# Performance work log

Measured on AMD Instinct MI355X. Metric: run time of the kernel, lower is better.

Reference implementation:

```python
import jax, jax.numpy as jnp
import numpy as np

N_NODES = 100000
N_EDGES = 1600000
HIDDEN = 128


def setup_inputs() -> dict:
    key = jax.random.key(0)
    k1, k2, k3, k4, k5 = jax.random.split(key, 5)
    probabilities = jax.random.uniform(k1, (N_EDGES,), dtype=jnp.float32)
    hidden = jax.random.normal(k2, (N_NODES, HIDDEN), dtype=jnp.float32)
    edge_index = jax.random.randint(k3, (2, N_EDGES), 0, N_NODES, dtype=jnp.int32)
    # nn.Linear(hidden_dim, hidden_dim): weight [out, in], bias [out]
    bound = 1.0 / np.sqrt(HIDDEN)
    lin_w = jax.random.uniform(k4, (HIDDEN, HIDDEN), minval=-bound, maxval=bound, dtype=jnp.float32)
    lin_b = jax.random.uniform(k5, (HIDDEN,), minval=-bound, maxval=bound, dtype=jnp.float32)
    return {"probabilities": probabilities, "hidden": hidden, "edge_index": edge_index,
            "lin_w": lin_w, "lin_b": lin_b}


def reference(probabilities, hidden, edge_index, lin_w, lin_b):
    # gather target-node hidden states: [E, H]
    target_hidden = hidden[edge_index[1]]
    # scale each message by its edge probability
    weighted_msg = target_hidden * probabilities[:, None]
    # scatter_add into source-node buckets: [N, H]
    aggregated = jax.ops.segment_sum(weighted_msg, edge_index[0], num_segments=hidden.shape[0])
    # trailing linear: y = aggregated @ W^T + b
    return aggregated @ lin_w.T + lin_b
```

## Files before the change

kernel.cpp:

```cpp
#include <hip/hip_runtime.h>

#define HIDDEN 128
#define NPB 64
#define CHUNK 4096
#define NBMAX 2048
#define CAP 1280

typedef __attribute__((ext_vector_type(8))) short bf16x8;
typedef __attribute__((ext_vector_type(4))) float f32x4;

static __device__ __forceinline__ ushort f2bf(float f) {
    uint u = __float_as_uint(f);
    uint r = (u + 0x7fffu + ((u >> 16) & 1u)) >> 16;
    return (ushort)r;
}

static __device__ __forceinline__ void split1(float f, ushort& h, ushort& l) {
    ushort hh = f2bf(f);
    float hf = __uint_as_float(((uint)hh) << 16);
    h = hh;
    l = f2bf(f - hf);
}

static __device__ __forceinline__ void splitt(float f, ushort& h, ushort& l) {
    uint u = __float_as_uint(f);
    h = (ushort)(u >> 16);
    l = f2bf(f - __uint_as_float(u & 0xffff0000u));
}

static __device__ __forceinline__ bf16x8 mkfrag(ushort4 a, ushort4 b) {
    bf16x8 f;
    f[0] = (short)a.x; f[1] = (short)a.y; f[2] = (short)a.z; f[3] = (short)a.w;
    f[4] = (short)b.x; f[5] = (short)b.y; f[6] = (short)b.z; f[7] = (short)b.w;
    return f;
}

__global__ __launch_bounds__(256) void bin_k(
    const int* __restrict__ ei, const float* __restrict__ prob,
    const float* __restrict__ W, int* __restrict__ gcur, int2* __restrict__ ed,
    ushort* __restrict__ wh, ushort* __restrict__ wl, int E, int NB, int HB)
{
    if ((int)blockIdx.x >= HB) {
        int i = ((int)blockIdx.x - HB) * 256 + threadIdx.x;
        ushort h, l;
        split1(W[i], h, l);
        wh[i] = h;
        wl[i] = l;
        return;
    }
    __shared__ int hist[NBMAX];
    __shared__ int base[NBMAX];
    const int t  = threadIdx.x;
    const int e0 = blockIdx.x * CHUNK;

    for (int i = t; i < NB; i += 256) hist[i] = 0;
    __syncthreads();

    int  bs[16];
    int2 pl[16];
    #pragma unroll
    for (int j = 0; j < 16; ++j) {
        int e = e0 + j * 256 + t;
        if (e < E) {
            int src = ei[e];
            int tgt = ei[E + e];
            int p15 = min((int)(prob[e] * 32768.0f + 0.5f), 32767);
            int b   = src >> 6;
            bs[j] = b;
            pl[j] = make_int2(tgt, ((src & (NPB - 1)) << 15) | p15);
            atomicAdd(&hist[b], 1);
        } else bs[j] = -1;
    }
    __syncthreads();

    for (int i = t; i < NB; i += 256) {
        int c = hist[i];
        base[i] = c ? (i * CAP + atomicAdd(&gcur[i], c)) : 0;
        hist[i] = 0;
    }
    __syncthreads();

    #pragma unroll
    for (int j = 0; j < 16; ++j) {
        if (bs[j] >= 0) {
            int r = atomicAdd(&hist[bs[j]], 1);
            ed[base[bs[j]] + r] = pl[j];
        }
    }
}

__global__ __launch_bounds__(256, 2) void gemm_mfma_k(
    const float* __restrict__ A, const ushort* __restrict__ wh,
    const ushort* __restrict__ wl, ushort* __restrict__ hp, int N)
{
    __shared__ ushort a_hi[128 * 128];
    __shared__ ushort a_lo[128 * 128];

    const int t  = threadIdx.x;
    const int n0 = blockIdx.x * 128;

    #pragma unroll
    for (int i = 0; i < 16; ++i) {
        int idx4 = t + 256 * i;
        int row  = idx4 >> 5;
        int kq   = idx4 & 31;
        int n    = n0 + row;
        float4 v = (n < N) ? ((const float4*)A)[(size_t)n * 32 + kq]
                           : make_float4(0.f, 0.f, 0.f, 0.f);
        ushort4 h, l;
        splitt(v.x, h.x, l.x);
        splitt(v.y, h.y, l.y);
        splitt(v.z, h.z, l.z);
        splitt(v.w, h.w, l.w);
        uint off = (uint)((row << 8) + (kq << 3)) ^ (uint)((row & 7) << 4);
        *(ushort4*)((char*)a_hi + off) = h;
        *(ushort4*)((char*)a_lo + off) = l;
    }

    const int w  = t >> 6;
    const int l  = t & 63;
    const int wr = w >> 1;
    const int wc = w & 1;
    const int lg = l >> 4;
    const int li = l & 15;

    bf16x8 wfh[4][4], wfl[4][4];
    #pragma unroll
    for (int c = 0; c < 4; ++c) {
        int o = wc * 64 + c * 16 + li;
        #pragma unroll
        for (int ks = 0; ks < 4; ++ks) {
            int kb = ks * 32 + lg * 4;
            const ushort* ph = wh + o * 128 + kb;
            const ushort* pl = wl + o * 128 + kb;
            ushort4 h0 = *(const ushort4*)(ph);
            ushort4 h1 = *(const ushort4*)(ph + 16);
            ushort4 l0 = *(const ushort4*)(pl);
            ushort4 l1 = *(const ushort4*)(pl + 16);
            wfh[c][ks] = mkfrag(h0, h1);
            wfl[c][ks] = mkfrag(l0, l1);
        }
    }

    f32x4 acc[4][4];
    #pragma unroll
    for (int m = 0; m < 4; ++m)
        #pragma unroll
        for (int c = 0; c < 4; ++c)
            acc[m][c] = (f32x4){0.f, 0.f, 0.f, 0.f};

    __syncthreads();

    #pragma unroll
    for (int ks = 0; ks < 4; ++ks) {
        int kb2 = (ks * 32 + lg * 4) * 2;
        #pragma unroll
        for (int m = 0; m < 4; ++m) {
            int row  = wr * 64 + m * 16 + li;
            uint bse = (uint)(row << 8);
            uint swz = (uint)((row & 7) << 4);
            uint o0  = (bse + kb2) ^ swz;
            uint o1  = (bse + kb2 + 32) ^ swz;
            ushort4 h0 = *(ushort4*)((char*)a_hi + o0);
            ushort4 h1 = *(ushort4*)((char*)a_hi + o1);
            ushort4 q0 = *(ushort4*)((char*)a_lo + o0);
            ushort4 q1 = *(ushort4*)((char*)a_lo + o1);
            bf16x8 ah = mkfrag(h0, h1);
            bf16x8 al = mkfrag(q0, q1);
            #pragma unroll
            for (int c = 0; c < 4; ++c) {
                acc[m][c] = __builtin_amdgcn_mfma_f32_16x16x32_bf16(ah, wfh[c][ks], acc[m][c], 0, 0, 0);
                acc[m][c] = __builtin_amdgcn_mfma_f32_16x16x32_bf16(ah, wfl[c][ks], acc[m][c], 0, 0, 0);
                acc[m][c] = __builtin_amdgcn_mfma_f32_16x16x32_bf16(al, wfh[c][ks], acc[m][c], 0, 0, 0);
            }
        }
    }

    #pragma unroll
    for (int m = 0; m < 4; ++m) {
        #pragma unroll
        for (int i = 0; i < 4; ++i) {
            int n = n0 + wr * 64 + m * 16 + lg * 4 + i;
            if (n < N) {
                ushort* dst = hp + (size_t)n * 128 + wc * 64 + li;
                #pragma unroll
                for (int c = 0; c < 4; ++c)
                    dst[c * 16] = f2bf(acc[m][c][i]);
            }
        }
    }
}

__global__ __launch_bounds__(256, 8) void agg_k(
    const int*  __restrict__ gcur,
    const int2* __restrict__ ed,
    const ushort* __restrict__ hp,
    const float* __restrict__ bias,
    float*       __restrict__ out,
    int N)
{
    __shared__ int2 buf[CAP];
    __shared__ int  hist[NPB];
    __shared__ int  hoff[NPB + 1];

    const int t   = threadIdx.x;
    const int b   = blockIdx.x;
    const int nb0 = b * NPB;
    const int beg = b * CAP;
    const int c   = min(gcur[b], CAP);

    if (t < NPB) hist[t] = 0;
    __syncthreads();

    for (int i = t; i < c; i += 256)
        atomicAdd(&hist[(ed[beg + i].y >> 15) & (NPB - 1)], 1);
    __syncthreads();

    if (t < NPB) {
        int x = hist[t];
        int v = x;
        #pragma unroll
        for (int d = 1; d < 64; d <<= 1) {
            int u = __shfl_up(v, d);
            if (t >= d) v += u;
        }
        hoff[t] = v - x;
        hist[t] = 0;
        if (t == NPB - 1) hoff[NPB] = v;
    }
    __syncthreads();

    for (int i = t; i < c; i += 256) {
        int2 e = ed[beg + i];
        int lo = (e.y >> 15) & (NPB - 1);
        int r  = atomicAdd(&hist[lo], 1);
        buf[hoff[lo] + r] = e;
    }
    __syncthreads();

    const int wv = t >> 6;
    const int l  = t & 63;
    const int eg = l >> 4;
    const int cs = l & 15;
    const uint4* hpq = (const uint4*)hp;
    const float ps = 1.0f / 32768.0f;
    const float2 bv = ((const float2*)bias)[cs * 4 + eg];

    for (int ln = wv; ln < NPB; ln += 4) {
        int n = nb0 + ln;
        if (n >= N) break;
        const int s = hoff[ln];
        const int e = hoff[ln + 1];

        float acc[8];
        #pragma unroll
        for (int k = 0; k < 8; ++k) acc[k] = 0.f;

        int i = s;
        for (; i + 8 <= e; i += 8) {
            int2 d0 = buf[i + eg];
            int2 d1 = buf[i + 4 + eg];
            uint4 q0 = hpq[(size_t)d0.x * 16 + cs];
            uint4 q1 = hpq[(size_t)d1.x * 16 + cs];
            float p0 = (float)(d0.y & 0x7fff) * ps;
            float p1 = (float)(d1.y & 0x7fff) * ps;
            uint u;
            u = q0.x; acc[0] += p0 * __uint_as_float(u << 16); acc[1] += p0 * __uint_as_float(u & 0xffff0000u);
            u = q0.y; acc[2] += p0 * __uint_as_float(u << 16); acc[3] += p0 * __uint_as_float(u & 0xffff0000u);
            u = q0.z; acc[4] += p0 * __uint_as_float(u << 16); acc[5] += p0 * __uint_as_float(u & 0xffff0000u);
            u = q0.w; acc[6] += p0 * __uint_as_float(u << 16); acc[7] += p0 * __uint_as_float(u & 0xffff0000u);
            u = q1.x; acc[0] += p1 * __uint_as_float(u << 16); acc[1] += p1 * __uint_as_float(u & 0xffff0000u);
            u = q1.y; acc[2] += p1 * __uint_as_float(u << 16); acc[3] += p1 * __uint_as_float(u & 0xffff0000u);
            u = q1.z; acc[4] += p1 * __uint_as_float(u << 16); acc[5] += p1 * __uint_as_float(u & 0xffff0000u);
            u = q1.w; acc[6] += p1 * __uint_as_float(u << 16); acc[7] += p1 * __uint_as_float(u & 0xffff0000u);
        }
        for (; i < e; i += 4) {
            int ei_ = i + eg;
            int2 d = (ei_ < e) ? buf[ei_] : make_int2(0, 0);
            uint4 q = hpq[(size_t)d.x * 16 + cs];
            float p = (float)(d.y & 0x7fff) * ps;
            uint u;
            u = q.x; acc[0] += p * __uint_as_float(u << 16); acc[1] += p * __uint_as_float(u & 0xffff0000u);
            u = q.y; acc[2] += p * __uint_as_float(u << 16); acc[3] += p * __uint_as_float(u & 0xffff0000u);
            u = q.z; acc[4] += p * __uint_as_float(u << 16); acc[5] += p * __uint_as_float(u & 0xffff0000u);
            u = q.w; acc[6] += p * __uint_as_float(u << 16); acc[7] += p * __uint_as_float(u & 0xffff0000u);
        }

        #pragma unroll
        for (int k = 0; k < 8; ++k) {
            float vv = acc[k];
            vv += __shfl_xor(vv, 16);
            vv += __shfl_xor(vv, 32);
            acc[k] = vv;
        }

        float2 r;
        r.x = acc[eg * 2]     + bv.x;
        r.y = acc[eg * 2 + 1] + bv.y;
        ((float2*)(out + (size_t)n * HIDDEN))[cs * 4 + eg] = r;
    }
}

extern "C" void kernel_launch(void* const* d_in, const int* in_sizes, int n_in,
                              void* d_out, int out_size, void* d_ws, size_t ws_size,
                              hipStream_t stream)
{
    const float* prob   = (const float*)d_in[0];
    const float* hidden = (const float*)d_in[1];
    const int*   ei     = (const int*)  d_in[2];
    const float* W      = (const float*)d_in[3];
    const float* bias   = (const float*)d_in[4];
    float*       out    = (float*)d_out;

    const int E  = in_sizes[0];
    const int N  = in_sizes[1] / HIDDEN;
    const int NB = (N + NPB - 1) / NPB;
    const int HB = (E + CHUNK - 1) / CHUNK;

    char* w = (char*)d_ws;
    int* gcur = (int*)w;
    size_t ib = ((size_t)NB * 4 + 255) & ~(size_t)255;
    int2*   ed = (int2*)(w + ib);
    ushort* hp = (ushort*)(w + ib + (size_t)NB * CAP * 8);
    ushort* wh = hp + (size_t)N * 128;
    ushort* wl = wh + 128 * 128;

    (void)hipMemsetAsync(gcur, 0, (size_t)NB * sizeof(int), stream);

    bin_k<<<HB + 64, 256, 0, stream>>>(ei, prob, W, gcur, ed, wh, wl, E, NB, HB);
    gemm_mfma_k<<<(N + 127) / 128, 256, 0, stream>>>(hidden, wh, wl, hp, N);
    agg_k<<<NB, 256, 0, stream>>>(gcur, ed, hp, bias, out, N);
}
```

Measured before the change: 254.5 us.

## Fuse edge binning and GEMM into one kernel, split W inline, unroll gather

Merges the edge-binning kernel and the MFMA GEMM kernel into a single launch. Each block first bins its edge chunk if its index is below BINB, then reuses the same shared memory for its GEMM tile. The W hi/lo split now happens inline per GEMM block instead of going through a separate workspace pass. The aggregation loop also gains a 16-edge unrolled step to keep more gathers in flight. This removes one kernel launch and lets binning overlap with GEMM, at the cost of serialising both phases inside the blocks that do both and slightly more register pressure.

```diff
diff --git a/kernel.cpp b/kernel.cpp
--- a/kernel.cpp
+++ b/kernel.cpp
@@ -15,13 +15,6 @@
     return (ushort)r;
 }
 
-static __device__ __forceinline__ void split1(float f, ushort& h, ushort& l) {
-    ushort hh = f2bf(f);
-    float hf = __uint_as_float(((uint)hh) << 16);
-    h = hh;
-    l = f2bf(f - hf);
-}
-
 static __device__ __forceinline__ void splitt(float f, ushort& h, ushort& l) {
     uint u = __float_as_uint(f);
     h = (ushort)(u >> 16);
@@ -35,68 +28,61 @@
     return f;
 }
 
-__global__ __launch_bounds__(256) void bin_k(
+__global__ __launch_bounds__(256, 2) void bg_k(
     const int* __restrict__ ei, const float* __restrict__ prob,
-    const float* __restrict__ W, int* __restrict__ gcur, int2* __restrict__ ed,
-    ushort* __restrict__ wh, ushort* __restrict__ wl, int E, int NB, int HB)
+    const float* __restrict__ A, const float* __restrict__ W,
+    int* __restrict__ gcur, int2* __restrict__ ed, ushort* __restrict__ hp,
+    int E, int N, int NB, int BINB, int GEMB)
 {
-    if ((int)blockIdx.x >= HB) {
-        int i = ((int)blockIdx.x - HB) * 256 + threadIdx.x;
-        ushort h, l;
-        split1(W[i], h, l);
-        wh[i] = h;
-        wl[i] = l;
-        return;
-    }
-    __shared__ int hist[NBMAX];
-    __shared__ int base[NBMAX];
-    const int t  = threadIdx.x;
-    const int e0 = blockIdx.x * CHUNK;
-
-    for (int i = t; i < NB; i += 256) hist[i] = 0;
-    __syncthreads();
-
-    int  bs[16];
-    int2 pl[16];
-    #pragma unroll
-    for (int j = 0; j < 16; ++j) {
-        int e = e0 + j * 256 + t;
-        if (e < E) {
-            int src = ei[e];
-            int tgt = ei[E + e];
-            int p15 = min((int)(prob[e] * 32768.0f + 0.5f), 32767);
-            int b   = src >> 6;
-            bs[j] = b;
-            pl[j] = make_int2(tgt, ((src & (NPB - 1)) << 15) | p15);
-            atomicAdd(&hist[b], 1);
-        } else bs[j] = -1;
-    }
-    __syncthreads();
-
-    for (int i = t; i < NB; i += 256) {
-        int c = hist[i];
-        base[i] = c ? (i * CAP + atomicAdd(&gcur[i], c)) : 0;
-        hist[i] = 0;
-    }
-    __syncthreads();
-
-    #pragma unroll
-    for (int j = 0; j < 16; ++j) {
-        if (bs[j] >= 0) {
-            int r = atomicAdd(&hist[bs[j]], 1);
-            ed[base[bs[j]] + r] = pl[j];
-        }
-    }
-}
-
-__global__ __launch_bounds__(256, 2) void gemm_mfma_k(
-    const float* __restrict__ A, const ushort* __restrict__ wh,
-    const ushort* __restrict__ wl, ushort* __restrict__ hp, int N)
-{
-    __shared__ ushort a_hi[128 * 128];
-    __shared__ ushort a_lo[128 * 128];
-
-    const int t  = threadIdx.x;
+    __shared__ char smem[65536];
+    const int t = threadIdx.x;
+
+    if ((int)blockIdx.x < BINB) {
+        int* hist = (int*)smem;
+        int* base = (int*)(smem + 4 * NBMAX);
+        const int e0 = blockIdx.x * CHUNK;
+
+        for (int i = t; i < NB; i += 256) hist[i] = 0;
+        __syncthreads();
+
+        int  bs[16];
+        int2 pl[16];
+        #pragma unroll
+        for (int j = 0; j < 16; ++j) {
+            int e = e0 + j * 256 + t;
+            if (e < E) {
+                int src = ei[e];
+                int tgt = ei[E + e];
+                int p15 = min((int)(prob[e] * 32768.0f + 0.5f), 32767);
+                int b   = src >> 6;
+                bs[j] = b;
+                pl[j] = make_int2(tgt, ((src & (NPB - 1)) << 15) | p15);
+                atomicAdd(&hist[b], 1);
+            } else bs[j] = -1;
+        }
+        __syncthreads();
+
+        for (int i = t; i < NB; i += 256) {
+            int c = hist[i];
+            base[i] = c ? (i * CAP + atomicAdd(&gcur[i], c)) : 0;
+            hist[i] = 0;
+        }
+        __syncthreads();
+
+        #pragma unroll
+        for (int j = 0; j < 16; ++j) {
+            if (bs[j] >= 0) {
+                int r = atomicAdd(&hist[bs[j]], 1);
+                ed[base[bs[j]] + r] = pl[j];
+            }
+        }
+        __syncthreads();
+    }
+
+    if ((int)blockIdx.x >= GEMB) return;
+    ushort* a_hi = (ushort*)smem;
+    ushort* a_lo = (ushort*)(smem + 32768);
+
     const int n0 = blockIdx.x * 128;
 
     #pragma unroll
@@ -131,12 +117,14 @@
         #pragma unroll
         for (int ks = 0; ks < 4; ++ks) {
             int kb = ks * 32 + lg * 4;
-            const ushort* ph = wh + o * 128 + kb;
-            const ushort* pl = wl + o * 128 + kb;
-            ushort4 h0 = *(const ushort4*)(ph);
-            ushort4 h1 = *(const ushort4*)(ph + 16);
-            ushort4 l0 = *(const ushort4*)(pl);
-            ushort4 l1 = *(const ushort4*)(pl + 16);
+            const float* pw = W + o * 128 + kb;
+            float4 w0 = *(const float4*)(pw);
+            float4 w1 = *(const float4*)(pw + 16);
+            ushort4 h0, l0, h1, l1;
+            splitt(w0.x, h0.x, l0.x); splitt(w0.y, h0.y, l0.y);
+            splitt(w0.z, h0.z, l0.z); splitt(w0.w, h0.w, l0.w);
+            splitt(w1.x, h1.x, l1.x); splitt(w1.y, h1.y, l1.y);
+            splitt(w1.z, h1.z, l1.z); splitt(w1.w, h1.w, l1.w);
             wfh[c][ks] = mkfrag(h0, h1);
             wfl[c][ks] = mkfrag(l0, l1);
         }
@@ -257,6 +245,37 @@
         for (int k = 0; k < 8; ++k) acc[k] = 0.f;
 
         int i = s;
+        for (; i + 16 <= e; i += 16) {
+            int2 d0 = buf[i + eg];
+            int2 d1 = buf[i + 4 + eg];
+            int2 d2 = buf[i + 8 + eg];
+            int2 d3 = buf[i + 12 + eg];
+            uint4 q0 = hpq[(size_t)d0.x * 16 + cs];
+            uint4 q1 = hpq[(size_t)d1.x * 16 + cs];
+            uint4 q2 = hpq[(size_t)d2.x * 16 + cs];
+            uint4 q3 = hpq[(size_t)d3.x * 16 + cs];
+            float p0 = (float)(d0.y & 0x7fff) * ps;
+            float p1 = (float)(d1.y & 0x7fff) * ps;
+            float p2 = (float)(d2.y & 0x7fff) * ps;
+            float p3 = (float)(d3.y & 0x7fff) * ps;
+            uint u;
+            u = q0.x; acc[0] += p0 * __uint_as_float(u << 16); acc[1] += p0 * __uint_as_float(u & 0xffff0000u);
+            u = q0.y; acc[2] += p0 * __uint_as_float(u << 16); acc[3] += p0 * __uint_as_float(u & 0xffff0000u);
+            u = q0.z; acc[4] += p0 * __uint_as_float(u << 16); acc[5] += p0 * __uint_as_float(u & 0xffff0000u);
+            u = q0.w; acc[6] += p0 * __uint_as_float(u << 16); acc[7] += p0 * __uint_as_float(u & 0xffff0000u);
+            u = q1.x; acc[0] += p1 * __uint_as_float(u << 16); acc[1] += p1 * __uint_as_float(u & 0xffff0000u);
+            u = q1.y; acc[2] += p1 * __uint_as_float(u << 16); acc[3] += p1 * __uint_as_float(u & 0xffff0000u);
+            u = q1.z; acc[4] += p1 * __uint_as_float(u << 16); acc[5] += p1 * __uint_as_float(u & 0xffff0000u);
+            u = q1.w; acc[6] += p1 * __uint_as_float(u << 16); acc[7] += p1 * __uint_as_float(u & 0xffff0000u);
+            u = q2.x; acc[0] += p2 * __uint_as_float(u << 16); acc[1] += p2 * __uint_as_float(u & 0xffff0000u);
+            u = q2.y; acc[2] += p2 * __uint_as_float(u << 16); acc[3] += p2 * __uint_as_float(u & 0xffff0000u);
+            u = q2.z; acc[4] += p2 * __uint_as_float(u << 16); acc[5] += p2 * __uint_as_float(u & 0xffff0000u);
+            u = q2.w; acc[6] += p2 * __uint_as_float(u << 16); acc[7] += p2 * __uint_as_float(u & 0xffff0000u);
+            u = q3.x; acc[0] += p3 * __uint_as_float(u << 16); acc[1] += p3 * __uint_as_float(u & 0xffff0000u);
+            u = q3.y; acc[2] += p3 * __uint_as_float(u << 16); acc[3] += p3 * __uint_as_float(u & 0xffff0000u);
+            u = q3.z; acc[4] += p3 * __uint_as_float(u << 16); acc[5] += p3 * __uint_as_float(u & 0xffff0000u);
+            u = q3.w; acc[6] += p3 * __uint_as_float(u << 16); acc[7] += p3 * __uint_as_float(u & 0xffff0000u);
+        }
         for (; i + 8 <= e; i += 8) {
             int2 d0 = buf[i + eg];
             int2 d1 = buf[i + 4 + eg];
@@ -312,22 +331,22 @@
     const float* bias   = (const float*)d_in[4];
     float*       out    = (float*)d_out;
 
-    const int E  = in_sizes[0];
-    const int N  = in_sizes[1] / HIDDEN;
-    const int NB = (N + NPB - 1) / NPB;
-    const int HB = (E + CHUNK - 1) / CHUNK;
+    const int E    = in_sizes[0];
+    const int N    = in_sizes[1] / HIDDEN;
+    const int NB   = (N + NPB - 1) / NPB;
+    const int BINB = (E + CHUNK - 1) / CHUNK;
+    const int GEMB = (N + 127) / 128;
+    const int GRID = (BINB > GEMB) ? BINB : GEMB;
 
     char* w = (char*)d_ws;
     int* gcur = (int*)w;
     size_t ib = ((size_t)NB * 4 + 255) & ~(size_t)255;
     int2*   ed = (int2*)(w + ib);
     ushort* hp = (ushort*)(w + ib + (size_t)NB * CAP * 8);
-    ushort* wh = hp + (size_t)N * 128;
-    ushort* wl = wh + 128 * 128;
 
     (void)hipMemsetAsync(gcur, 0, (size_t)NB * sizeof(int), stream);
 
-    bin_k<<<HB + 64, 256, 0, stream>>>(ei, prob, W, gcur, ed, wh, wl, E, NB, HB);
-    gemm_mfma_k<<<(N + 127) / 128, 256, 0, stream>>>(hidden, wh, wl, hp, N);
+    bg_k<<<GRID, 256, 0, stream>>>(ei, prob, hidden, W, gcur, ed, hp,
+                                   E, N, NB, BINB, GEMB);
     agg_k<<<NB, 256, 0, stream>>>(gcur, ed, hp, bias, out, N);
 }
```

Result: faster. 246.2 us (-3.3%).
